# Kernel tuning notes

Measured on AMD Instinct MI355X. Metric: run time of the kernel, lower is better.

Reference implementation:

```python
import jax, jax.numpy as jnp
import numpy as np
import itertools
from itertools import combinations

N_QUBITS = 6
DIM = 2 ** N_QUBITS            # 64
N_GEN = DIM ** 2 - 1           # 4095 (SU(2^n) generators)
K_LOCAL = 2
OBS_DIM = 2 ** K_LOCAL         # 4
WIRE_GROUPS = [list(c) for c in combinations(range(N_QUBITS), K_LOCAL)]
N_OBS = len(WIRE_GROUPS)       # 15
N_OFF = OBS_DIM * (OBS_DIM - 1) // 2  # 6
CHUNK_DIM = 512
T_EMB = 256
HID = 256
BATCH = 512

# lower-triangle (i>j) flat ordering used by create_Hermitian: c = i*(i-1)/2 + j
_TRI_R = np.array([i for i in range(1, OBS_DIM) for j in range(i)])
_TRI_C = np.array([j for i in range(1, OBS_DIM) for j in range(i)])
_DIAG = np.arange(OBS_DIM - 1)  # diag slots 0..N-2 get 2*D[1..N-1]; last diag is 0


def _pauli_basis():
    """Lexicographic Pauli words on N_QUBITS qubits, identity excluded -> (N_GEN, DIM, DIM)."""
    I = np.eye(2, dtype=np.complex64)
    X = np.array([[0, 1], [1, 0]], dtype=np.complex64)
    Y = np.array([[0, -1j], [1j, 0]], dtype=np.complex64)
    Z = np.array([[1, 0], [0, -1]], dtype=np.complex64)
    P1 = {'I': I, 'X': X, 'Y': Y, 'Z': Z}
    out = np.empty((N_GEN, DIM, DIM), dtype=np.complex64)
    k = 0
    for word in itertools.product('IXYZ', repeat=N_QUBITS):
        if all(c == 'I' for c in word):
            continue
        m = np.array([[1.0 + 0j]], dtype=np.complex64)
        for c in word:
            m = np.kron(m, P1[c])
        out[k] = m
        k += 1
    return jnp.asarray(out)


def setup_inputs() -> dict:
    key = jax.random.key(0)
    ks = jax.random.split(key, 12)
    inp = {
        'x': jax.random.normal(ks[0], (BATCH, CHUNK_DIM + T_EMB), dtype=jnp.float32),
        # enc_proj: Linear(768,256) -> SiLU -> Linear(256,4095)
        'W1': jax.random.normal(ks[1], (CHUNK_DIM + T_EMB, HID), dtype=jnp.float32) * 0.02,
        'b1': jnp.zeros((HID,), dtype=jnp.float32),
        'W2': jax.random.normal(ks[2], (HID, N_GEN), dtype=jnp.float32) * 0.02,
        'b2': jnp.zeros((N_GEN,), dtype=jnp.float32),
        # ANO Hermitian params (std=2.0 per torch init)
        'Aoff': jax.random.normal(ks[3], (N_OBS, N_OFF), dtype=jnp.float32) * 2.0,
        'Boff': jax.random.normal(ks[4], (N_OBS, N_OFF), dtype=jnp.float32) * 2.0,
        'Ddiag': jax.random.normal(ks[5], (N_OBS, OBS_DIM), dtype=jnp.float32) * 2.0,
        # vel_head: Linear(15,256) -> SiLU -> Linear(256,512)
        'Wv1': jax.random.normal(ks[6], (N_OBS, HID), dtype=jnp.float32) * 0.02,
        'bv1': jnp.zeros((HID,), dtype=jnp.float32),
        'Wv2': jax.random.normal(ks[7], (HID, CHUNK_DIM), dtype=jnp.float32) * 0.02,
        'bv2': jnp.zeros((CHUNK_DIM,), dtype=jnp.float32),
        'pauli': _pauli_basis(),  # fixed SU(2^n) generator basis (constant)
    }
    return inp


def _build_H(Aoff, Boff, Ddiag):
    """Batched create_Hermitian: (N_OBS, 4, 4) complex. h + h^H semantics."""
    H = jnp.zeros((N_OBS, OBS_DIM, OBS_DIM), dtype=jnp.complex64)
    off = Aoff.astype(jnp.complex64) + 1j * Boff.astype(jnp.complex64)
    H = H.at[:, _TRI_R, _TRI_C].set(off)
    H = H + jnp.conj(jnp.swapaxes(H, -1, -2))
    H = H.at[:, _DIAG, _DIAG].set((2.0 * Ddiag[:, 1:]).astype(jnp.complex64))
    return H


def _forward(x, W1, b1, W2, b2, Aoff, Boff, Ddiag, Wv1, bv1, Wv2, bv2, pauli):
    B = x.shape[0]
    # enc_proj MLP -> SU(2^n) angles theta (B, 4095)
    enc = jax.nn.silu(x @ W1 + b1) @ W2 + b2
    # SpecialUnitary: U = exp(i * sum_m theta_m P_m); apply to |0...0> via eigh of the
    # Hermitian effective generator H_eff = sum_m theta_m P_m.
    H_eff = jnp.einsum('bm,mij->bij', enc.astype(jnp.complex64), pauli)  # (B, 64, 64)
    lam, V = jnp.linalg.eigh(H_eff)
    # psi = V @ diag(exp(i*lam)) @ V^dag @ e0 ; (V^dag e0)_j = conj(V[0, j])
    psi = jnp.einsum('bij,bj->bi', V, jnp.exp(1j * lam.astype(jnp.complex64)) * jnp.conj(V[:, 0, :]))
    H = _build_H(Aoff, Boff, Ddiag)  # (15, 4, 4)
    psi_t = psi.reshape((B,) + (2,) * N_QUBITS)
    q = []
    for w, (a, b) in enumerate(WIRE_GROUPS):
        # bring wires (a,b) to front (wire order: first wire is most significant bit)
        pg = jnp.moveaxis(psi_t, (1 + a, 1 + b), (1, 2)).reshape(B, OBS_DIM, -1)
        # <H> = tr(rho H), rho_kl = sum_r psi[k,r] conj(psi[l,r])
        q.append(jnp.einsum('bkr,blr,lk->b', pg, jnp.conj(pg), H[w]).real)
    q = jnp.stack(q, axis=1).astype(jnp.float32)  # (B, 15)
    return jax.nn.silu(q @ Wv1 + bv1) @ Wv2 + bv2  # (B, 512)


def reference(x, W1, b1, W2, b2, Aoff, Boff, Ddiag, Wv1, bv1, Wv2, bv2, pauli):
    return _forward(x, W1, b1, W2, b2, Aoff, Boff, Ddiag, Wv1, bv1, Wv2, bv2, pauli)
```

## Files before the change

### kernel.cpp

```cpp
#include <hip/hip_runtime.h>
#include <hip/hip_bf16.h>

#define BATCH   512
#define INDIM   768
#define HID     256
#define NGEN    4095
#define NGENP   4096
#define NOBS    15
#define OUTDIM  512
#define DIM     64

typedef __hip_bfloat16 bf16;

__device__ int      g_isf32;
__device__ float    g_theta[(size_t)BATCH*NGENP];
__device__ float    g_h[(size_t)BATCH*HID];
__device__ float    g_W2p[(size_t)HID*NGENP];
__device__ float    g_b2p[NGENP];

__device__ __forceinline__ float tof(bf16 v){ return __bfloat162float(v); }
__device__ __forceinline__ float silu(float x){ return x / (1.f + __expf(-x)); }
__device__ __forceinline__ float blo(unsigned u){ return __uint_as_float(u<<16); }
__device__ __forceinline__ float bhi(unsigned u){ return __uint_as_float(u & 0xFFFF0000u); }

template<bool F32>
__device__ __forceinline__ float LD(const void* p, size_t i){
  if(F32) return ((const float*)p)[i];
  else    return tof(((const bf16*)p)[i]);
}

__device__ __forceinline__ unsigned spread6(unsigned x){
  return (x&1u) | ((x&2u)<<1) | ((x&4u)<<2) | ((x&8u)<<3) | ((x&16u)<<4) | ((x&32u)<<5);
}

__device__ __forceinline__ bool detect_f32(const unsigned* __restrict__ w1raw, int* red){
  const int t = threadIdx.x & (blockDim.x-1);
  const int lane = t & 63, wav = t >> 6;
  int c = 0;
  for(int i=t;i<1024;i+=(int)blockDim.x){
    unsigned ub = (w1raw[i]>>8) & 0x7Fu;
    if(ub>=0x30u && ub<=0x3Fu) c++;
  }
  #pragma unroll
  for(int s=1;s<64;s<<=1) c += __shfl_xor(c, s);
  if(lane==0) red[wav] = c;
  __syncthreads();
  int nw = (int)blockDim.x >> 6;
  int tot = 0;
  for(int w=0;w<nw;w++) tot += red[w];
  return tot < 512;
}

__constant__ int c_WA[15] = {0,0,0,0,0,1,1,1,1,2,2,2,3,3,4};
__constant__ int c_WB[15] = {1,2,3,4,5,2,3,4,5,3,4,5,4,5,5};
__constant__ int c_Lt[6]  = {1,2,2,3,3,3};
__constant__ int c_Kt[6]  = {0,0,1,0,1,2};

template<bool F32>
__device__ void prep_body(const void* __restrict__ x, const void* __restrict__ W1,
                          const void* __restrict__ b1, const void* __restrict__ W2,
                          const void* __restrict__ b2, float (*xl)[4]){
  const int t = threadIdx.x;
  const size_t gid = (size_t)blockIdx.x*256 + t;
  const size_t stride = (size_t)gridDim.x*256;

  for(size_t i=gid;i<(size_t)HID*NGENP;i+=stride){
    size_t k = i>>12, c = i&4095;
    g_W2p[i] = (c<NGEN) ? LD<F32>(W2,k*NGEN+c) : 0.f;
  }
  for(size_t i=gid;i<NGENP;i+=stride) g_b2p[i] = (i<NGEN) ? LD<F32>(b2,i) : 0.f;

  if(blockIdx.x < BATCH/4){
    const int b0 = blockIdx.x*4;
    for(int i=t;i<4*INDIM;i+=256){
      int r = i/INDIM, k = i - r*INDIM;
      xl[k][r] = LD<F32>(x,(size_t)(b0+r)*INDIM + k);
    }
    __syncthreads();
    const int rh = t>>7, tc = t&127;
    float a00=0.f,a01=0.f,a10=0.f,a11=0.f;
    for(int k0=0;k0<INDIM;k0+=8){
      #pragma unroll
      for(int u=0;u<8;u++){
        float wvx, wvy;
        if(F32){
          float2 wv = *(const float2*)&((const float*)W1)[(size_t)(k0+u)*HID + 2*tc];
          wvx = wv.x; wvy = wv.y;
        } else {
          unsigned w = ((const unsigned*)W1)[(size_t)(k0+u)*(HID/2) + tc];
          wvx = blo(w); wvy = bhi(w);
        }
        float2 xv = *(const float2*)&xl[k0+u][2*rh];
        a00 += xv.x*wvx; a01 += xv.x*wvy;
        a10 += xv.y*wvx; a11 += xv.y*wvy;
      }
    }
    const float bb0 = LD<F32>(b1,2*tc), bb1 = LD<F32>(b1,2*tc+1);
    g_h[(size_t)(b0+2*rh+0)*HID + 2*tc+0] = silu(a00+bb0);
    g_h[(size_t)(b0+2*rh+0)*HID + 2*tc+1] = silu(a01+bb1);
    g_h[(size_t)(b0+2*rh+1)*HID + 2*tc+0] = silu(a10+bb0);
    g_h[(size_t)(b0+2*rh+1)*HID + 2*tc+1] = silu(a11+bb1);
  }
}

__global__ __launch_bounds__(256) void k_prep(const void* x,const void* W1,const void* b1,
                                              const void* W2,const void* b2){
  __shared__ __align__(16) float xl[INDIM][4];
  __shared__ int red[4];
  bool isf32 = detect_f32((const unsigned*)W1, red);
  if(blockIdx.x==0 && threadIdx.x==0) g_isf32 = isf32 ? 1 : 0;
  if(isf32) prep_body<true >(x,W1,b1,W2,b2,xl);
  else      prep_body<false>(x,W1,b1,W2,b2,xl);
}

__global__ __launch_bounds__(256) void k_enc2(){
  __shared__ __align__(16) float hl[HID][8];
  const int t  = threadIdx.x;
  const int b0 = (blockIdx.x>>2)*8;
  const int c0 = (blockIdx.x&3)*1024;
  for(int i=t;i<8*HID;i+=256){
    int r = i>>8, k = i&255;
    hl[k][r] = g_h[(size_t)(b0+r)*HID + k];
  }
  __syncthreads();
  const int col = c0 + 4*t;
  const float* Wbase = g_W2p + col;
  float4 bv = *(const float4*)&g_b2p[col];
  float acc[8][4];
  #pragma unroll
  for(int r=0;r<8;r++){ acc[r][0]=bv.x; acc[r][1]=bv.y; acc[r][2]=bv.z; acc[r][3]=bv.w; }

  float4 wA[8], wB[8];
  #pragma unroll
  for(int u=0;u<8;u++) wA[u] = *(const float4*)&Wbase[(size_t)u*NGENP];

  for(int k0=0;k0<HID;k0+=16){
    #pragma unroll
    for(int u=0;u<8;u++) wB[u] = *(const float4*)&Wbase[(size_t)(k0+8+u)*NGENP];
    #pragma unroll
    for(int u=0;u<8;u++){
      float4 wv = wA[u];
      float4 h0 = *(const float4*)&hl[k0+u][0];
      float4 h1 = *(const float4*)&hl[k0+u][4];
      acc[0][0]+=h0.x*wv.x; acc[0][1]+=h0.x*wv.y; acc[0][2]+=h0.x*wv.z; acc[0][3]+=h0.x*wv.w;
      acc[1][0]+=h0.y*wv.x; acc[1][1]+=h0.y*wv.y; acc[1][2]+=h0.y*wv.z; acc[1][3]+=h0.y*wv.w;
      acc[2][0]+=h0.z*wv.x; acc[2][1]+=h0.z*wv.y; acc[2][2]+=h0.z*wv.z; acc[2][3]+=h0.z*wv.w;
      acc[3][0]+=h0.w*wv.x; acc[3][1]+=h0.w*wv.y; acc[3][2]+=h0.w*wv.z; acc[3][3]+=h0.w*wv.w;
      acc[4][0]+=h1.x*wv.x; acc[4][1]+=h1.x*wv.y; acc[4][2]+=h1.x*wv.z; acc[4][3]+=h1.x*wv.w;
      acc[5][0]+=h1.y*wv.x; acc[5][1]+=h1.y*wv.y; acc[5][2]+=h1.y*wv.z; acc[5][3]+=h1.y*wv.w;
      acc[6][0]+=h1.z*wv.x; acc[6][1]+=h1.z*wv.y; acc[6][2]+=h1.z*wv.z; acc[6][3]+=h1.z*wv.w;
      acc[7][0]+=h1.w*wv.x; acc[7][1]+=h1.w*wv.y; acc[7][2]+=h1.w*wv.z; acc[7][3]+=h1.w*wv.w;
    }
    if(k0+16 < HID){
      #pragma unroll
      for(int u=0;u<8;u++) wA[u] = *(const float4*)&Wbase[(size_t)(k0+16+u)*NGENP];
    }
    #pragma unroll
    for(int u=0;u<8;u++){
      float4 wv = wB[u];
      float4 h0 = *(const float4*)&hl[k0+8+u][0];
      float4 h1 = *(const float4*)&hl[k0+8+u][4];
      acc[0][0]+=h0.x*wv.x; acc[0][1]+=h0.x*wv.y; acc[0][2]+=h0.x*wv.z; acc[0][3]+=h0.x*wv.w;
      acc[1][0]+=h0.y*wv.x; acc[1][1]+=h0.y*wv.y; acc[1][2]+=h0.y*wv.z; acc[1][3]+=h0.y*wv.w;
      acc[2][0]+=h0.z*wv.x; acc[2][1]+=h0.z*wv.y; acc[2][2]+=h0.z*wv.z; acc[2][3]+=h0.z*wv.w;
      acc[3][0]+=h0.w*wv.x; acc[3][1]+=h0.w*wv.y; acc[3][2]+=h0.w*wv.z; acc[3][3]+=h0.w*wv.w;
      acc[4][0]+=h1.x*wv.x; acc[4][1]+=h1.x*wv.y; acc[4][2]+=h1.x*wv.z; acc[4][3]+=h1.x*wv.w;
      acc[5][0]+=h1.y*wv.x; acc[5][1]+=h1.y*wv.y; acc[5][2]+=h1.y*wv.z; acc[5][3]+=h1.y*wv.w;
      acc[6][0]+=h1.z*wv.x; acc[6][1]+=h1.z*wv.y; acc[6][2]+=h1.z*wv.z; acc[6][3]+=h1.z*wv.w;
      acc[7][0]+=h1.w*wv.x; acc[7][1]+=h1.w*wv.y; acc[7][2]+=h1.w*wv.z; acc[7][3]+=h1.w*wv.w;
    }
  }
  #pragma unroll
  for(int r=0;r<8;r++){
    float4 o = make_float4(acc[r][0],acc[r][1],acc[r][2],acc[r][3]);
    *(float4*)&g_theta[(size_t)(b0+r)*NGENP + col] = o;
  }
}

template<bool F32>
__device__ void state_body(const void* __restrict__ Aoff, const void* __restrict__ Boff,
                           const void* __restrict__ Ddiag,
                           const void* __restrict__ Wv1, const void* __restrict__ bv1,
                           const void* __restrict__ Wv2, const void* __restrict__ bv2,
                           void* __restrict__ out, char* sm){
  float*  th   = (float*)sm;
  float*  HH   = (float*)(sm + 16384);
  typedef float2 rep_t[66];
  rep_t*  vrA  = (rep_t*)sm;
  rep_t*  vrB  = (rep_t*)(sm + 2112);
  float2* ps   = (float2*)(sm + 4224);
  float2* coef = (float2*)(sm + 4736);
  float*  rs   = (float*)(sm + 6016);
  float*  qacc = (float*)(sm + 6272);
  float*  s_inva = (float*)(sm + 6336);
  int*    s_K    = (int*)(sm + 6340);
  float*  s_aG   = (float*)(sm + 6344);
  float*  hl   = (float*)(sm + 6400);
  float (*part)[64][8] = (float(*)[64][8])(sm + 7424);
  float*  n11  = (float*)(sm + 15616);
  float*  n12  = (float*)(sm + 15872);

  const int b = blockIdx.x, t = threadIdx.x;
  for(int m=t;m<NGEN;m+=256) th[m] = g_theta[(size_t)b*NGENP+m];
  __syncthreads();

  const int lane = t & 63, wav = t >> 6;
  for(int it=0; it<16; ++it){
    int d = (it<<2) | wav;
    unsigned td = (unsigned)(lane & d);
    unsigned tn = (unsigned)(lane & ~d) & 63u;
    unsigned w  = spread6((unsigned)d) + spread6(td) + 3u*spread6(tn);
    float thv = (w==0u) ? 0.f : th[w-1u];
    int ny = __popc(td) & 3;
    float gr = (ny==0)?  thv : (ny==2 ? -thv : 0.f);
    float gi = (ny==1)? -thv : (ny==3 ?  thv : 0.f);
    #pragma unroll
    for(int s=1;s<64;s<<=1){
      float pr = __shfl_xor(gr, s);
      float pi = __shfl_xor(gi, s);
      if(lane & s){ gr = pr - gr; gi = pi - gi; }
      else        { gr = gr + pr; gi = gi + pi; }
    }
    int j = lane ^ d;
    HH[lane*132 + 2*j]   = gr;
    HH[lane*132 + 2*j+1] = gi;
  }
  __syncthreads();

  const int i = t >> 2, c = t & 3, j0 = c*16;
  float hreg[32];
  float rsum = 0.f;
  #pragma unroll
  for(int jj=0;jj<16;jj+=2){
    float4 hv = *(const float4*)&HH[i*132 + 2*(j0+jj)];
    hreg[2*jj+0]=hv.x; hreg[2*jj+1]=hv.y; hreg[2*jj+2]=hv.z; hreg[2*jj+3]=hv.w;
    rsum += fabsf(hv.x)+fabsf(hv.y)+fabsf(hv.z)+fabsf(hv.w);
  }
  rsum += __shfl_xor(rsum,1);
  rsum += __shfl_xor(rsum,2);
  if(c==0) rs[i] = rsum;
  __syncthreads();

  if(t==0){
    float aG = 0.5f;
    for(int r=0;r<DIM;r++) aG = fmaxf(aG, rs[r]);
    *s_aG = aG;
  }
  __syncthreads();
  const float aG    = *s_aG;
  const float invaG = 1.f/aG;

  {
    rep_t* pv1 = vrA;
    rep_t* pv0 = vrB;
    if(t < DIM){
      float2 e0v = make_float2(t==0?1.f:0.f, 0.f);
      #pragma unroll
      for(int cc=0;cc<4;cc++) pv1[cc][t] = e0v;
    }
    __syncthreads();
    for(int m=1;m<=12;++m){
      const float* vb = (const float*)&pv1[c][0];
      float yr=0.f, yi=0.f;
      #pragma unroll
      for(int jj=0;jj<16;jj+=2){
        float4 xv = *(const float4*)&vb[2*(j0+jj)];
        float hr0=hreg[2*jj], hi0=hreg[2*jj+1], hr1=hreg[2*jj+2], hi1=hreg[2*jj+3];
        yr += hr0*xv.x - hi0*xv.y;
        yi += hr0*xv.y + hi0*xv.x;
        yr += hr1*xv.z - hi1*xv.w;
        yi += hr1*xv.w + hi1*xv.z;
      }
      yr += __shfl_xor(yr,1); yr += __shfl_xor(yr,2);
      yi += __shfl_xor(yi,1); yi += __shfl_xor(yi,2);
      if(c==0){
        float vnr = invaG*yr, vni = invaG*yi;
        float2 vn = make_float2(vnr, vni);
        #pragma unroll
        for(int cc=0;cc<4;cc++) pv0[cc][i] = vn;
        if(m==11) n11[i] = vnr*vnr + vni*vni;
        if(m==12) n12[i] = vnr*vnr + vni*vni;
      }
      __syncthreads();
      rep_t* tmp = pv0; pv0 = pv1; pv1 = tmp;
    }
  }

  if(t==0){
    float s11=0.f, s12=0.f;
    for(int r=0;r<DIM;r++){ s11 += n11[r]; s12 += n12[r]; }
    float a = aG;
    if(s11 > 1e-30f){
      float ratio = sqrtf(s12/s11);
      float ap = 1.35f * ratio * aG;
      a = fminf(aG, fmaxf(ap, 0.5f));
    }
    int K = (int)ceilf(a + 6.f*cbrtf(a) + 10.f);
    if(K>150) K=150;
    float bkp=0.f, bk=1e-35f, snorm=0.f;
    for(int k=K+12;k>=1;--k){
      float bkm = (2.f*(float)k/a)*bk - bkp;
      int n = k-1;
      if(n<=K) coef[n].x = bkm;
      if((n&1)==0) snorm += (n==0?1.f:2.f)*bkm;
      bkp = bk; bk = bkm;
    }
    float invs = 1.f/snorm;
    for(int n=0;n<=K;n++){
      float cv = coef[n].x*invs*(n==0?1.f:2.f);
      int p = n&3;
      float cr = (p==0)? cv : (p==2 ? -cv : 0.f);
      float ci = (p==1)? cv : (p==3 ? -cv : 0.f);
      coef[n] = make_float2(cr,ci);
    }
    *s_K = K;
    *s_inva = 1.f/a;
  }
  __syncthreads();
  const float inva = *s_inva;
  const int K = *s_K;

  rep_t* v0r = vrA;
  rep_t* v1r = vrB;
  if(t < DIM){
    float2 w1 = make_float2(HH[t*132+0]*inva, HH[t*132+1]*inva);
    float2 e0 = make_float2(t==0?1.f:0.f, 0.f);
    #pragma unroll
    for(int cc=0;cc<4;cc++){ v0r[cc][t] = e0; v1r[cc][t] = w1; }
    float2 c0 = coef[0], c1 = coef[1];
    float2 p;
    p.x = (t==0?c0.x:0.f) + c1.x*w1.x - c1.y*w1.y;
    p.y = (t==0?c0.y:0.f) + c1.x*w1.y + c1.y*w1.x;
    ps[t] = p;
  }
  __syncthreads();

  for(int k=2;k<=K;k++){
    const float* vb = (const float*)&v1r[c][0];
    float yr=0.f, yi=0.f;
    #pragma unroll
    for(int jj=0;jj<16;jj+=2){
      float4 xv = *(const float4*)&vb[2*(j0+jj)];
      float hr0=hreg[2*jj], hi0=hreg[2*jj+1], hr1=hreg[2*jj+2], hi1=hreg[2*jj+3];
      yr += hr0*xv.x - hi0*xv.y;
      yi += hr0*xv.y + hi0*xv.x;
      yr += hr1*xv.z - hi1*xv.w;
      yi += hr1*xv.w + hi1*xv.z;
    }
    yr += __shfl_xor(yr,1); yr += __shfl_xor(yr,2);
    yi += __shfl_xor(yi,1); yi += __shfl_xor(yi,2);
    if(c==0){
      float2 vm = v0r[0][i];
      float2 vn = make_float2(2.f*inva*yr - vm.x, 2.f*inva*yi - vm.y);
      #pragma unroll
      for(int cc=0;cc<4;cc++) v0r[cc][i] = vn;
      float2 ck = coef[k];
      float2 p = ps[i];
      p.x += ck.x*vn.x - ck.y*vn.y;
      p.y += ck.x*vn.y + ck.y*vn.x;
      ps[i] = p;
    }
    __syncthreads();
    rep_t* tmp = v0r; v0r = v1r; v1r = tmp;
  }

  if(t<NOBS) qacc[t]=0.f;
  __syncthreads();

  if(t<150){
    int w = t/10, s = t%10;
    int posA = 5 - c_WA[w], posB = 5 - c_WB[w];
    float contrib = 0.f;
    bool have = false;
    if(s<4){
      int kk = s;
      if(kk<3){
        float val = 0.f;
        for(int r=0;r<16;r++){
          int idx = (((kk>>1)&1)<<posA) | ((kk&1)<<posB);
          int rb = 3;
          #pragma unroll
          for(int p=5;p>=0;--p){
            if(p==posA || p==posB) continue;
            idx |= ((r>>rb)&1)<<p;
            rb--;
          }
          float2 pv = ps[idx];
          val += pv.x*pv.x + pv.y*pv.y;
        }
        contrib = val*2.f*LD<F32>(Ddiag, w*4 + kk + 1);
        have = true;
      }
    } else {
      int cc = s-4;
      int l = c_Lt[cc], kk = c_Kt[cc];
      float zr=0.f, zi=0.f;
      for(int r=0;r<16;r++){
        int idxk = (((kk>>1)&1)<<posA) | ((kk&1)<<posB);
        int idxl = (((l >>1)&1)<<posA) | ((l &1)<<posB);
        int rb = 3;
        #pragma unroll
        for(int p=5;p>=0;--p){
          if(p==posA || p==posB) continue;
          int bit = (r>>rb)&1;
          idxk |= bit<<p; idxl |= bit<<p;
          rb--;
        }
        float2 pk = ps[idxk], pl = ps[idxl];
        zr += pk.x*pl.x + pk.y*pl.y;
        zi += pk.y*pl.x - pk.x*pl.y;
      }
      contrib = 2.f*(zr*LD<F32>(Aoff,w*6+cc) - zi*LD<F32>(Boff,w*6+cc));
      have = true;
    }
    if(have) atomicAdd(&qacc[w], contrib);
  }
  __syncthreads();

  if(!F32){
    {
      float acc = tof(((const bf16*)bv1)[t]);
      #pragma unroll
      for(int k=0;k<NOBS;k++) acc += qacc[k]*tof(((const bf16*)Wv1)[k*HID+t]);
      hl[t] = silu(acc);
    }
    __syncthreads();
    const int rg = t >> 6;
    const uint4* w2v = (const uint4*)Wv2;
    float a8[8] = {0.f,0.f,0.f,0.f,0.f,0.f,0.f,0.f};
    for(int kk=0; kk<64; kk+=8){
      uint4 wv[8];
      #pragma unroll
      for(int u=0;u<8;u++) wv[u] = w2v[(size_t)(rg*64+kk+u)*64 + lane];
      #pragma unroll
      for(int u=0;u<8;u++){
        float hk = hl[rg*64+kk+u];
        a8[0] += hk*blo(wv[u].x); a8[1] += hk*bhi(wv[u].x);
        a8[2] += hk*blo(wv[u].y); a8[3] += hk*bhi(wv[u].y);
        a8[4] += hk*blo(wv[u].z); a8[5] += hk*bhi(wv[u].z);
        a8[6] += hk*blo(wv[u].w); a8[7] += hk*bhi(wv[u].w);
      }
    }
    #pragma unroll
    for(int j=0;j<8;j++) part[rg][lane][j] = a8[j];
    __syncthreads();
    {
      int cA = 2*t, cB = 2*t+1;
      float vA = tof(((const bf16*)bv2)[cA]);
      float vB = tof(((const bf16*)bv2)[cB]);
      #pragma unroll
      for(int r2=0;r2<4;r2++){
        vA += part[r2][cA>>3][cA&7];
        vB += part[r2][cB>>3][cB&7];
      }
      bf16 ha = __float2bfloat16(vA), hb = __float2bfloat16(vB);
      unsigned pw = (unsigned)(*(unsigned short*)&ha) |
                    ((unsigned)(*(unsigned short*)&hb)<<16);
      ((unsigned*)out)[(size_t)b*(OUTDIM/2) + t] = pw;
    }
  } else {
    {
      float acc = ((const float*)bv1)[t];
      #pragma unroll
      for(int k=0;k<NOBS;k++) acc += qacc[k]*((const float*)Wv1)[k*HID+t];
      hl[t] = silu(acc);
    }
    __syncthreads();
    #pragma unroll
    for(int oo=0;oo<2;oo++){
      int o = t + oo*256;
      float s0=0.f;
      for(int k=0;k<HID;k++) s0 += hl[k]*((const float*)Wv2)[(size_t)k*OUTDIM+o];
      ((float*)out)[(size_t)b*OUTDIM+o] = ((const float*)bv2)[o] + s0;
    }
  }
}

__global__ __launch_bounds__(256) void k_state(const void* Aoff,const void* Boff,const void* Dd,
                                               const void* Wv1,const void* bv1,
                                               const void* Wv2,const void* bv2, void* out){
  __shared__ __align__(16) char sm[50176];
  if(g_isf32) state_body<true >(Aoff,Boff,Dd,Wv1,bv1,Wv2,bv2,out,sm);
  else        state_body<false>(Aoff,Boff,Dd,Wv1,bv1,Wv2,bv2,out,sm);
}

extern "C" void kernel_launch(void* const* d_in, const int* in_sizes, int n_in,
                              void* d_out, int out_size, void* d_ws, size_t ws_size,
                              hipStream_t stream){
  const void* x    = d_in[0];
  const void* W1   = d_in[1];
  const void* b1   = d_in[2];
  const void* W2   = d_in[3];
  const void* b2   = d_in[4];
  const void* Aoff = d_in[5];
  const void* Boff = d_in[6];
  const void* Dd   = d_in[7];
  const void* Wv1  = d_in[8];
  const void* bv1  = d_in[9];
  const void* Wv2  = d_in[10];
  const void* bv2  = d_in[11];

  k_prep <<<1024,256,0,stream>>>(x,W1,b1,W2,b2);
  k_enc2 <<<256,256,0,stream>>>();
  k_state<<<BATCH,256,0,stream>>>(Aoff,Boff,Dd,Wv1,bv1,Wv2,bv2,d_out);
}
```

Before: 246.8 us.

## Keep W2 as bf16 in enc2 and estimate spectral radius from theta norm

The bf16 path now repacks W2 into a padded 16-bit buffer and unpacks it inside the encoder GEMM, which halves the weight bytes read compared with the fp32 copy. The state kernel drops the 12-step power iteration used to estimate the spectral radius for the Chebyshev expansion. It uses a bound of 2.3 times the Frobenius norm of theta, accumulated while theta is loaded into shared memory, capped by the row-sum bound. The heuristic bound may give a larger or smaller polynomial degree than before, which changes both cost and accuracy.

```diff
diff --git a/kernel.cpp b/kernel.cpp
--- a/kernel.cpp
+++ b/kernel.cpp
@@ -16,12 +16,14 @@
 __device__ float    g_theta[(size_t)BATCH*NGENP];
 __device__ float    g_h[(size_t)BATCH*HID];
 __device__ float    g_W2p[(size_t)HID*NGENP];
+__device__ unsigned short g_W2h[(size_t)HID*NGENP];
 __device__ float    g_b2p[NGENP];
 
 __device__ __forceinline__ float tof(bf16 v){ return __bfloat162float(v); }
 __device__ __forceinline__ float silu(float x){ return x / (1.f + __expf(-x)); }
 __device__ __forceinline__ float blo(unsigned u){ return __uint_as_float(u<<16); }
 __device__ __forceinline__ float bhi(unsigned u){ return __uint_as_float(u & 0xFFFF0000u); }
+__device__ __forceinline__ float hs(unsigned short u){ return __uint_as_float(((unsigned)u)<<16); }
 
 template<bool F32>
 __device__ __forceinline__ float LD(const void* p, size_t i){
@@ -64,9 +66,24 @@
   const size_t gid = (size_t)blockIdx.x*256 + t;
   const size_t stride = (size_t)gridDim.x*256;
 
-  for(size_t i=gid;i<(size_t)HID*NGENP;i+=stride){
-    size_t k = i>>12, c = i&4095;
-    g_W2p[i] = (c<NGEN) ? LD<F32>(W2,k*NGEN+c) : 0.f;
+  if(F32){
+    for(size_t i=gid;i<(size_t)HID*NGENP;i+=stride){
+      size_t k = i>>12, c = i&4095;
+      g_W2p[i] = (c<NGEN) ? LD<F32>(W2,k*NGEN+c) : 0.f;
+    }
+  } else {
+    const size_t N2 = (size_t)HID*NGEN/2;
+    const unsigned* src = (const unsigned*)W2;
+    for(size_t i2=gid;i2<N2;i2+=stride){
+      unsigned v = src[i2];
+      size_t e0 = 2*i2;
+      size_t k  = e0/NGEN, c = e0 - k*NGEN;
+      g_W2h[k*NGENP + c] = (unsigned short)(v & 0xFFFFu);
+      size_t c1 = c+1, k1 = k;
+      if(c1==NGEN){ c1 = 0; k1 = k+1; }
+      if(k1<HID) g_W2h[k1*NGENP + c1] = (unsigned short)(v>>16);
+    }
+    for(size_t k=gid;k<HID;k+=stride) g_W2h[k*NGENP + NGEN] = 0;
   }
   for(size_t i=gid;i<NGENP;i+=stride) g_b2p[i] = (i<NGEN) ? LD<F32>(b2,i) : 0.f;
 
@@ -113,8 +130,8 @@
   else      prep_body<false>(x,W1,b1,W2,b2,xl);
 }
 
-__global__ __launch_bounds__(256) void k_enc2(){
-  __shared__ __align__(16) float hl[HID][8];
+template<bool F32>
+__device__ void enc2_body(float (*hl)[8]){
   const int t  = threadIdx.x;
   const int b0 = (blockIdx.x>>2)*8;
   const int c0 = (blockIdx.x&3)*1024;
@@ -124,22 +141,37 @@
   }
   __syncthreads();
   const int col = c0 + 4*t;
-  const float* Wbase = g_W2p + col;
   float4 bv = *(const float4*)&g_b2p[col];
   float acc[8][4];
   #pragma unroll
   for(int r=0;r<8;r++){ acc[r][0]=bv.x; acc[r][1]=bv.y; acc[r][2]=bv.z; acc[r][3]=bv.w; }
 
+  const float* WbaseF = g_W2p + col;
+  const uint2* WbaseH = (const uint2*)(g_W2h + col);
+
   float4 wA[8], wB[8];
-  #pragma unroll
-  for(int u=0;u<8;u++) wA[u] = *(const float4*)&Wbase[(size_t)u*NGENP];
+  uint2  hA[8], hB[8];
+  if(F32){
+    #pragma unroll
+    for(int u=0;u<8;u++) wA[u] = *(const float4*)&WbaseF[(size_t)u*NGENP];
+  } else {
+    #pragma unroll
+    for(int u=0;u<8;u++) hA[u] = WbaseH[(size_t)u*(NGENP/4)];
+  }
+
+  #define UNPACK(W_, H_, U_) float4 W_; if(F32){ W_ = (U_)[u]; } else { uint2 hh=(H_)[u]; W_=make_float4(blo(hh.x),bhi(hh.x),blo(hh.y),bhi(hh.y)); }
 
   for(int k0=0;k0<HID;k0+=16){
-    #pragma unroll
-    for(int u=0;u<8;u++) wB[u] = *(const float4*)&Wbase[(size_t)(k0+8+u)*NGENP];
+    if(F32){
+      #pragma unroll
+      for(int u=0;u<8;u++) wB[u] = *(const float4*)&WbaseF[(size_t)(k0+8+u)*NGENP];
+    } else {
+      #pragma unroll
+      for(int u=0;u<8;u++) hB[u] = WbaseH[(size_t)(k0+8+u)*(NGENP/4)];
+    }
     #pragma unroll
     for(int u=0;u<8;u++){
-      float4 wv = wA[u];
+      UNPACK(wv, hA, wA);
       float4 h0 = *(const float4*)&hl[k0+u][0];
       float4 h1 = *(const float4*)&hl[k0+u][4];
       acc[0][0]+=h0.x*wv.x; acc[0][1]+=h0.x*wv.y; acc[0][2]+=h0.x*wv.z; acc[0][3]+=h0.x*wv.w;
@@ -152,12 +184,17 @@
       acc[7][0]+=h1.w*wv.x; acc[7][1]+=h1.w*wv.y; acc[7][2]+=h1.w*wv.z; acc[7][3]+=h1.w*wv.w;
     }
     if(k0+16 < HID){
-      #pragma unroll
-      for(int u=0;u<8;u++) wA[u] = *(const float4*)&Wbase[(size_t)(k0+16+u)*NGENP];
+      if(F32){
+        #pragma unroll
+        for(int u=0;u<8;u++) wA[u] = *(const float4*)&WbaseF[(size_t)(k0+16+u)*NGENP];
+      } else {
+        #pragma unroll
+        for(int u=0;u<8;u++) hA[u] = WbaseH[(size_t)(k0+16+u)*(NGENP/4)];
+      }
     }
     #pragma unroll
     for(int u=0;u<8;u++){
-      float4 wv = wB[u];
+      UNPACK(wv, hB, wB);
       float4 h0 = *(const float4*)&hl[k0+8+u][0];
       float4 h1 = *(const float4*)&hl[k0+8+u][4];
       acc[0][0]+=h0.x*wv.x; acc[0][1]+=h0.x*wv.y; acc[0][2]+=h0.x*wv.z; acc[0][3]+=h0.x*wv.w;
@@ -170,11 +207,18 @@
       acc[7][0]+=h1.w*wv.x; acc[7][1]+=h1.w*wv.y; acc[7][2]+=h1.w*wv.z; acc[7][3]+=h1.w*wv.w;
     }
   }
+  #undef UNPACK
   #pragma unroll
   for(int r=0;r<8;r++){
     float4 o = make_float4(acc[r][0],acc[r][1],acc[r][2],acc[r][3]);
     *(float4*)&g_theta[(size_t)(b0+r)*NGENP + col] = o;
   }
+}
+
+__global__ __launch_bounds__(256) void k_enc2(){
+  __shared__ __align__(16) float hl[HID][8];
+  if(g_isf32) enc2_body<true >(hl);
+  else        enc2_body<false>(hl);
 }
 
 template<bool F32>
@@ -194,14 +238,17 @@
   float*  qacc = (float*)(sm + 6272);
   float*  s_inva = (float*)(sm + 6336);
   int*    s_K    = (int*)(sm + 6340);
-  float*  s_aG   = (float*)(sm + 6344);
   float*  hl   = (float*)(sm + 6400);
   float (*part)[64][8] = (float(*)[64][8])(sm + 7424);
-  float*  n11  = (float*)(sm + 15616);
-  float*  n12  = (float*)(sm + 15872);
+  float*  s2p  = (float*)(sm + 15616);
 
   const int b = blockIdx.x, t = threadIdx.x;
-  for(int m=t;m<NGEN;m+=256) th[m] = g_theta[(size_t)b*NGENP+m];
+  float s2l = 0.f;
+  for(int m=t;m<NGEN;m+=256){
+    float v = g_theta[(size_t)b*NGENP+m];
+    th[m] = v;
+    s2l += v*v;
+  }
   __syncthreads();
 
   const int lane = t & 63, wav = t >> 6;
@@ -239,62 +286,16 @@
   rsum += __shfl_xor(rsum,1);
   rsum += __shfl_xor(rsum,2);
   if(c==0) rs[i] = rsum;
+  #pragma unroll
+  for(int s=1;s<64;s<<=1) s2l += __shfl_xor(s2l, s);
+  if(lane==0) s2p[wav] = s2l;
   __syncthreads();
 
   if(t==0){
     float aG = 0.5f;
     for(int r=0;r<DIM;r++) aG = fmaxf(aG, rs[r]);
-    *s_aG = aG;
-  }
-  __syncthreads();
-  const float aG    = *s_aG;
-  const float invaG = 1.f/aG;
-
-  {
-    rep_t* pv1 = vrA;
-    rep_t* pv0 = vrB;
-    if(t < DIM){
-      float2 e0v = make_float2(t==0?1.f:0.f, 0.f);
-      #pragma unroll
-      for(int cc=0;cc<4;cc++) pv1[cc][t] = e0v;
-    }
-    __syncthreads();
-    for(int m=1;m<=12;++m){
-      const float* vb = (const float*)&pv1[c][0];
-      float yr=0.f, yi=0.f;
-      #pragma unroll
-      for(int jj=0;jj<16;jj+=2){
-        float4 xv = *(const float4*)&vb[2*(j0+jj)];
-        float hr0=hreg[2*jj], hi0=hreg[2*jj+1], hr1=hreg[2*jj+2], hi1=hreg[2*jj+3];
-        yr += hr0*xv.x - hi0*xv.y;
-        yi += hr0*xv.y + hi0*xv.x;
-        yr += hr1*xv.z - hi1*xv.w;
-        yi += hr1*xv.w + hi1*xv.z;
-      }
-      yr += __shfl_xor(yr,1); yr += __shfl_xor(yr,2);
-      yi += __shfl_xor(yi,1); yi += __shfl_xor(yi,2);
-      if(c==0){
-        float vnr = invaG*yr, vni = invaG*yi;
-        float2 vn = make_float2(vnr, vni);
-        #pragma unroll
-        for(int cc=0;cc<4;cc++) pv0[cc][i] = vn;
-        if(m==11) n11[i] = vnr*vnr + vni*vni;
-        if(m==12) n12[i] = vnr*vnr + vni*vni;
-      }
-      __syncthreads();
-      rep_t* tmp = pv0; pv0 = pv1; pv1 = tmp;
-    }
-  }
-
-  if(t==0){
-    float s11=0.f, s12=0.f;
-    for(int r=0;r<DIM;r++){ s11 += n11[r]; s12 += n12[r]; }
-    float a = aG;
-    if(s11 > 1e-30f){
-      float ratio = sqrtf(s12/s11);
-      float ap = 1.35f * ratio * aG;
-      a = fminf(aG, fmaxf(ap, 0.5f));
-    }
+    float s2tot = s2p[0]+s2p[1]+s2p[2]+s2p[3];
+    float a = fminf(aG, fmaxf(2.3f*sqrtf(s2tot), 0.5f));
     int K = (int)ceilf(a + 6.f*cbrtf(a) + 10.f);
     if(K>150) K=150;
     float bkp=0.f, bk=1e-35f, snorm=0.f;
```

After: 258.2 us. 4.6% more time.
